# Kernel tuning notes

Hardware: AMD Instinct MI355X
Metric: run time of the kernel (lower is better)

Reference implementation:

```python
import jax, jax.numpy as jnp
import numpy as np

NEG_BIG = -1e10  # K.switch(A==0, -1e10, 0) mask value
LRELU_ALPHA = 0.2


def setup_inputs() -> dict:
    key = jax.random.key(0)
    kX, kA, kW, kS, kN = jax.random.split(key, 5)
    B, N, F, H, F_ = 4, 2048, 256, 8, 64
    X = jax.random.normal(kX, (B, N, F), dtype=jnp.float32)
    A = jax.random.bernoulli(kA, 0.05, (B, N, N)).astype(jnp.float32)
    eye = jnp.eye(N, dtype=jnp.float32)[None]
    A = jnp.maximum(A, eye)
    W = jax.random.normal(kW, (H, F, F_), dtype=jnp.float32) * 0.05
    a_self = jax.random.normal(kS, (H, F_), dtype=jnp.float32) * 0.05
    a_neigh = jax.random.normal(kN, (H, F_), dtype=jnp.float32) * 0.05
    return {"X": X, "A": A, "W": W, "a_self": a_self, "a_neigh": a_neigh}


def reference(X, A, W, a_self, a_neigh):
    # per-head linear transform, vectorized over heads: [B,H,N,F_]
    h = jnp.einsum('bnf,hfo->bhno', X, W)
    att_s = jnp.einsum('bhno,ho->bhn', h, a_self)    # attn_for_self
    att_n = jnp.einsum('bhno,ho->bhn', h, a_neigh)   # attn_for_neighs
    # broadcast-add -> dense NxN scores per head, LeakyReLU(0.2)
    dense = att_s[:, :, :, None] + att_n[:, :, None, :]          # [B,H,N,N]
    dense = jax.nn.leaky_relu(dense, LRELU_ALPHA)
    mask = jnp.where(A == 0.0, NEG_BIG, 0.0)[:, None, :, :]      # [B,1,N,N]
    attn = jax.nn.softmax(dense + mask, axis=-1)
    # weighted aggregation (dropout is identity at inference / attn_dropout=0)
    out = jnp.einsum('bhnm,bhmo->bhno', attn, h)                 # [B,H,N,F_]
    out = jax.nn.relu(out)                                       # per-head activation (concat mode)
    B, H, N, F_ = out.shape
    return out.transpose(0, 2, 1, 3).reshape(B, N, H * F_)       # concat heads
```

## Files before the change

### kernel.cpp

```cpp
#include <hip/hip_runtime.h>


constexpr int GN  = 2048;
constexpr int GHF = 512;

using sh8    = __attribute__((ext_vector_type(8))) short;
using hf8    = __attribute__((ext_vector_type(8))) _Float16;
using us4g   = __attribute__((ext_vector_type(4))) unsigned short;
using f32x4g = __attribute__((ext_vector_type(4))) float;
using u32x4g = __attribute__((ext_vector_type(4))) unsigned int;
using i32x4g = __attribute__((ext_vector_type(4))) int;

__device__ inline float gat_bf2f(unsigned short u) {
    union { unsigned int i; float f; } c; c.i = ((unsigned int)u) << 16; return c.f;
}
__device__ inline unsigned short gat_f2bf(float f) {
    union { float f; unsigned int i; } c; c.f = f;
    return (unsigned short)((c.i + 0x7fffu + ((c.i >> 16) & 1u)) >> 16);
}
__device__ inline unsigned short gat_f2h(float f) {
    _Float16 h = (_Float16)f;
    union { _Float16 h; unsigned short u; } c; c.h = h; return c.u;
}
__device__ inline float gat_h2f(unsigned short u) {
    union { _Float16 h; unsigned short u; } c; c.u = u; return (float)c.h;
}
__device__ inline int gat_isf32(const float* __restrict__ Aw) {
    float a = Aw[0];
    return (a == 0.0f) || (a == 1.0f);
}
__device__ inline unsigned int gat_enc(float f) {
    union { float f; unsigned int u; } c; c.f = f;
    return (c.u & 0x80000000u) ? ~c.u : (c.u | 0x80000000u);
}
__device__ inline float gat_dec(unsigned int e) {
    union { float f; unsigned int u; } c;
    c.u = (e & 0x80000000u) ? (e & 0x7fffffffu) : ~e;
    return c.f;
}
__device__ inline size_t gat_hswz_idx(int o, int j) {
    int jc = j >> 5, quad = (j >> 3) & 3, e = j & 7;
    int lane = quad * 16 + (o & 15);
    return (((size_t)(jc * 4 + (o >> 4))) * 64 + lane) * 8 + e;
}
__device__ inline size_t gat_wf_idx(int hh, int k, int col) {
    int kg = k >> 5, quad = (k >> 3) & 3, e = k & 7;
    int ct = col >> 4, lrw = col & 15;
    return ((((size_t)hh * 8 + kg) * 4 + ct) * 64 + (quad * 16 + lrw)) * 8 + e;
}

__global__ void GraphAttention_62981400429165_kernel() {}

constexpr size_t OFF_HS   = 256;
constexpr size_t OFF_ATTS = OFF_HS   + 8388608;
constexpr size_t OFF_EF   = OFF_ATTS + 262144;
constexpr size_t OFF_E5F  = OFF_EF   + 131072;
constexpr size_t OFF_MASK = OFF_E5F  + 131072;
constexpr size_t OFF_MAXN = OFF_MASK + 2097152;
constexpr size_t OFF_WC   = OFF_MAXN + 256;

__global__ __launch_bounds__(256) void k_mask_conv(const void* __restrict__ Araw,
                                                   const void* __restrict__ Wraw,
                                                   unsigned long long* __restrict__ mask,
                                                   unsigned int* __restrict__ maxn_enc,
                                                   unsigned short* __restrict__ Wf) {
    int tid = threadIdx.x, blk = blockIdx.x;
    int isf = gat_isf32((const float*)Araw);
    if (blk < 8192) {
        if (blk == 0 && tid < 32) maxn_enc[tid] = 0u;
        size_t i8 = ((size_t)blk * 256 + tid) * 8;
        unsigned int byte = 0;
        if (isf) {
            f32x4g v0 = *(const f32x4g*)((const float*)Araw + i8);
            f32x4g v1 = *(const f32x4g*)((const float*)Araw + i8 + 4);
#pragma unroll
            for (int e = 0; e < 4; e++) {
                byte |= (v0[e] != 0.0f ? 1u : 0u) << e;
                byte |= (v1[e] != 0.0f ? 1u : 0u) << (e + 4);
            }
        } else {
            u32x4g v = *(const u32x4g*)((const unsigned short*)Araw + i8);
#pragma unroll
            for (int w = 0; w < 4; w++) {
                byte |= ((v[w] & 0xffffu) != 0u ? 1u : 0u) << (2 * w);
                byte |= ((v[w] >> 16) != 0u ? 1u : 0u) << (2 * w + 1);
            }
        }
        ((unsigned char*)mask)[i8 >> 3] = (unsigned char)byte;
    } else {
        int gid = (blk - 8192) * 256 + tid;
        int lane = gid & 63, ct = (gid >> 6) & 3, kg = (gid >> 8) & 7, hh = gid >> 11;
        int quad = lane >> 4, lrw = lane & 15;
        int col = ct * 16 + lrw;
        us4g lo, hi;
#pragma unroll
        for (int e = 0; e < 8; e++) {
            int k = kg * 32 + quad * 8 + e;
            size_t src = (size_t)hh * 16384 + (size_t)k * 64 + col;
            unsigned short v = isf ? gat_f2bf(((const float*)Wraw)[src])
                                   : ((const unsigned short*)Wraw)[src];
            if (e < 4) lo[e] = v; else hi[e - 4] = v;
        }
        *(us4g*)&Wf[(size_t)gid * 8]     = lo;
        *(us4g*)&Wf[(size_t)gid * 8 + 4] = hi;
    }
}

constexpr int LDW = 264;
__global__ __launch_bounds__(256) void k_gemm1(const void* __restrict__ Xraw,
                                               const unsigned short* __restrict__ Wf,
                                               const void* __restrict__ aSraw,
                                               const void* __restrict__ aNraw,
                                               const float* __restrict__ Aw,
                                               unsigned short* __restrict__ hswz,
                                               float* __restrict__ att_s,
                                               unsigned short* __restrict__ Ef,
                                               unsigned short* __restrict__ E5f,
                                               unsigned int* __restrict__ maxn_enc) {
    int blk = blockIdx.x;
    int bh = blk >> 5, it = blk & 31;
    int b = bh >> 3, hh = bh & 7;
    int isf = gat_isf32(Aw);
#if defined(__gfx950__)
    __shared__ unsigned short CtT[64 * LDW];
    int wave = threadIdx.x >> 6, lane = threadIdx.x & 63;
    int lrw = lane & 15, quad = lane >> 4;
    int row0 = it * 64 + wave * 16;
    const unsigned short* wfh = Wf + (size_t)hh * 16384 + lane * 8;
    size_t xbase = ((size_t)(b * GN) + row0 + lrw) * 256;
    f32x4g acc[4] = {};
#pragma unroll 2
    for (int kg = 0; kg < 8; kg++) {
        sh8 a;
        if (isf) {
            const float* xp = (const float*)Xraw + xbase + kg * 32 + quad * 8;
            f32x4g x0 = *(const f32x4g*)xp;
            f32x4g x1 = *(const f32x4g*)(xp + 4);
            unsigned int w0_, w1_, w2_, w3_;
            asm("v_cvt_pk_bf16_f32 %0, %1, %2" : "=v"(w0_) : "v"(x0[0]), "v"(x0[1]));
            asm("v_cvt_pk_bf16_f32 %0, %1, %2" : "=v"(w1_) : "v"(x0[2]), "v"(x0[3]));
            asm("v_cvt_pk_bf16_f32 %0, %1, %2" : "=v"(w2_) : "v"(x1[0]), "v"(x1[1]));
            asm("v_cvt_pk_bf16_f32 %0, %1, %2" : "=v"(w3_) : "v"(x1[2]), "v"(x1[3]));
            i32x4g aw = {(int)w0_, (int)w1_, (int)w2_, (int)w3_};
            a = *(sh8*)&aw;
        } else {
            a = *(const sh8*)((const unsigned short*)Xraw + xbase + kg * 32 + quad * 8);
        }
        const unsigned short* wp = wfh + kg * 2048;
        sh8 w0 = *(const sh8*)&wp[0];
        sh8 w1 = *(const sh8*)&wp[512];
        sh8 w2 = *(const sh8*)&wp[1024];
        sh8 w3 = *(const sh8*)&wp[1536];
        acc[0] = __builtin_amdgcn_mfma_f32_16x16x32_bf16(a, w0, acc[0], 0, 0, 0);
        acc[1] = __builtin_amdgcn_mfma_f32_16x16x32_bf16(a, w1, acc[1], 0, 0, 0);
        acc[2] = __builtin_amdgcn_mfma_f32_16x16x32_bf16(a, w2, acc[2], 0, 0, 0);
        acc[3] = __builtin_amdgcn_mfma_f32_16x16x32_bf16(a, w3, acc[3], 0, 0, 0);
    }
    float as_l[4], an_l[4];
#pragma unroll
    for (int ct = 0; ct < 4; ct++) {
        int col = hh * 64 + ct * 16 + lrw;
        as_l[ct] = isf ? ((const float*)aSraw)[col] : gat_bf2f(((const unsigned short*)aSraw)[col]);
        an_l[ct] = isf ? ((const float*)aNraw)[col] : gat_bf2f(((const unsigned short*)aNraw)[col]);
    }
    float wmax = -3e38f;
#pragma unroll
    for (int r = 0; r < 4; r++) {
        float ps = acc[0][r] * as_l[0] + acc[1][r] * as_l[1]
                 + acc[2][r] * as_l[2] + acc[3][r] * as_l[3];
        float pn = acc[0][r] * an_l[0] + acc[1][r] * an_l[1]
                 + acc[2][r] * an_l[2] + acc[3][r] * an_l[3];
        for (int off = 1; off < 16; off <<= 1) {
            ps += __shfl_xor(ps, off);
            pn += __shfl_xor(pn, off);
        }
        int row = row0 + quad * 4 + r;
        if (lrw == 0) {
            att_s[bh * GN + row] = ps;
            float pnc = fminf(pn, 10.0f);
            Ef[bh * GN + row]  = gat_f2h(__expf(pnc));
            E5f[bh * GN + row] = gat_f2h(__expf(0.2f * pnc));
        }
        wmax = fmaxf(wmax, pn);
    }
    wmax = fmaxf(wmax, __shfl_xor(wmax, 16));
    wmax = fmaxf(wmax, __shfl_xor(wmax, 32));
    if (lane == 0) atomicMax(&maxn_enc[bh], gat_enc(wmax));
#pragma unroll
    for (int ct = 0; ct < 4; ct++) {
        int o = ct * 16 + lrw;
        int nloc = wave * 16 + quad * 4;
        us4g v;
        v[0] = gat_f2h(acc[ct][0]);
        v[1] = gat_f2h(acc[ct][1]);
        v[2] = gat_f2h(acc[ct][2]);
        v[3] = gat_f2h(acc[ct][3]);
        *(us4g*)&CtT[o * LDW + nloc] = v;
    }
    __syncthreads();
#pragma unroll
    for (int k = 0; k < 2; k++) {
        int id = k * 256 + threadIdx.x;
        int ln = id & 63, t = id >> 6;
        int jc_loc = t >> 2, ct = t & 3;
        int lrw2 = ln & 15, quad2 = ln >> 4;
        int o = ct * 16 + lrw2;
        int nloc = jc_loc * 32 + quad2 * 8;
        sh8 v = *(const sh8*)&CtT[o * LDW + nloc];
        size_t dst = ((((size_t)(bh * 64 + it * 2 + jc_loc)) * 4 + ct) * 64 + ln) * 8;
        *(sh8*)&hswz[dst] = v;
    }
#else
    if (threadIdx.x < 64) {
        int row = it * 64 + threadIdx.x;
        float hrow[64];
        for (int col = 0; col < 64; col++) {
            float sacc = 0.f;
            for (int k = 0; k < 256; k++) {
                float xv = isf ? ((const float*)Xraw)[((size_t)(b * GN) + row) * 256 + k]
                               : gat_bf2f(((const unsigned short*)Xraw)[((size_t)(b * GN) + row) * 256 + k]);
                sacc += xv * gat_bf2f(Wf[gat_wf_idx(hh, k, col)]);
            }
            hrow[col] = sacc;
        }
        size_t base = (size_t)bh * 64 * GN;
        for (int col = 0; col < 64; col++)
            hswz[base + gat_hswz_idx(col, row)] = gat_f2h(hrow[col]);
        float ps = 0.f, pn = 0.f;
        for (int col = 0; col < 64; col++) {
            float as = isf ? ((const float*)aSraw)[hh * 64 + col] : gat_bf2f(((const unsigned short*)aSraw)[hh * 64 + col]);
            float an = isf ? ((const float*)aNraw)[hh * 64 + col] : gat_bf2f(((const unsigned short*)aNraw)[hh * 64 + col]);
            ps += hrow[col] * as;
            pn += hrow[col] * an;
        }
        att_s[bh * GN + row] = ps;
        float pnc = fminf(pn, 10.0f);
        Ef[bh * GN + row]  = gat_f2h(__expf(pnc));
        E5f[bh * GN + row] = gat_f2h(__expf(0.2f * pnc));
        atomicMax(&maxn_enc[bh], gat_enc(pn));
    }
#endif
}

__global__ __launch_bounds__(256, 2) void k_attn_av(const unsigned int* __restrict__ mask32,
                                                    const unsigned short* __restrict__ hswz,
                                                    const float* __restrict__ att_s,
                                                    const unsigned short* __restrict__ Ef,
                                                    const unsigned short* __restrict__ E5f,
                                                    const unsigned int* __restrict__ maxn_enc,
                                                    const float* __restrict__ Aw,
                                                    void* __restrict__ outv) {
    int blk = blockIdx.x;
    int bh = blk & 31, it = blk >> 5;
    int b = bh >> 3, hh = bh & 7;
    int i0 = it * 64;
    int tid = threadIdx.x;
    int isf = gat_isf32(Aw);
    float maxn = gat_dec(maxn_enc[bh]);
#if defined(__gfx950__)
    int wave = tid >> 6, lane = tid & 63, lrw = lane & 15, quad = lane >> 4;
    int kq = quad * 8;
    int j0 = wave * 512;
    const unsigned short* hs = hswz + ((size_t)(bh * 64) + wave * 16) * 2048 + lane * 8;
    const unsigned int* Eu  = (const unsigned int*)Ef  + (size_t)bh * 1024;
    const unsigned int* E5u = (const unsigned int*)E5f + (size_t)bh * 1024;
    unsigned int k1p[4], k2p[4];
    const unsigned int* mrf[4];
#pragma unroll
    for (int f = 0; f < 4; f++) {
        int row = i0 + f * 16 + lrw;
        float s = att_s[bh * GN + row];
        float z = s + maxn;
        float c = fmaxf(z, 0.2f * z);
        k1p[f] = (unsigned int)gat_f2h(__expf(s - c)) * 0x00010001u;
        k2p[f] = (unsigned int)gat_f2h(__expf(0.2f * s - c)) * 0x00010001u;
        mrf[f] = mask32 + ((size_t)(b * GN) + row) * 64 + wave * 16;
    }
    f32x4g acc[4][4] = {};
    f32x4g accl[4] = {};
    hf8 ones;
#pragma unroll
    for (int e = 0; e < 8; e++) ones[e] = (_Float16)1.0f;

#pragma unroll 1
    for (int jg = 0; jg < 4; jg++) {
        u32x4g m0 = *(const u32x4g*)&mrf[0][jg * 4];
        u32x4g m1 = *(const u32x4g*)&mrf[1][jg * 4];
        u32x4g m2 = *(const u32x4g*)&mrf[2][jg * 4];
        u32x4g m3 = *(const u32x4g*)&mrf[3][jg * 4];
#pragma unroll
        for (int sj = 0; sj < 4; sj++) {
            int jc = jg * 4 + sj;
            int jh = ((j0 + jc * 32) >> 1) + quad * 4;
            u32x4g Ep  = *(const u32x4g*)&Eu[jh];
            u32x4g E5p = *(const u32x4g*)&E5u[jh];
            const unsigned short* hp = hs + jc * 2048;
            hf8 b0 = *(const hf8*)&hp[0];
            hf8 b1 = *(const hf8*)&hp[512];
            hf8 b2 = *(const hf8*)&hp[1024];
            hf8 b3 = *(const hf8*)&hp[1536];
            unsigned int wfm[4];
            wfm[0] = m0[sj] >> kq;
            wfm[1] = m1[sj] >> kq;
            wfm[2] = m2[sj] >> kq;
            wfm[3] = m3[sj] >> kq;
#pragma unroll
            for (int f = 0; f < 4; f++) {
                i32x4g fa;
#pragma unroll
                for (int pp = 0; pp < 4; pp++) {
                    unsigned int ew = Ep[pp], e5w = E5p[pp];
                    unsigned int a0, a1, mx;
                    asm("v_pk_mul_f16 %0, %1, %2" : "=v"(a0) : "v"(k1p[f]), "v"(ew));
                    asm("v_pk_mul_f16 %0, %1, %2" : "=v"(a1) : "v"(k2p[f]), "v"(e5w));
                    asm("v_pk_max_f16 %0, %1, %2" : "=v"(mx) : "v"(a0), "v"(a1));
                    unsigned int s0 = (unsigned int)__builtin_amdgcn_sbfe((int)wfm[f], 2u * pp, 1u);
                    unsigned int s1 = (unsigned int)__builtin_amdgcn_sbfe((int)wfm[f], 2u * pp + 1u, 1u);
                    fa[pp] = (int)(mx & ((s0 & 0x0000FFFFu) | (s1 & 0xFFFF0000u)));
                }
                hf8 af = *(hf8*)&fa;
                acc[f][0] = __builtin_amdgcn_mfma_f32_16x16x32_f16(af, b0, acc[f][0], 0, 0, 0);
                acc[f][1] = __builtin_amdgcn_mfma_f32_16x16x32_f16(af, b1, acc[f][1], 0, 0, 0);
                acc[f][2] = __builtin_amdgcn_mfma_f32_16x16x32_f16(af, b2, acc[f][2], 0, 0, 0);
                acc[f][3] = __builtin_amdgcn_mfma_f32_16x16x32_f16(af, b3, acc[f][3], 0, 0, 0);
                accl[f]   = __builtin_amdgcn_mfma_f32_16x16x32_f16(af, ones, accl[f], 0, 0, 0);
            }
        }
    }
    __shared__ float lred[4 * 64];
    __shared__ float lsum[64];
    __shared__ float red[4 * 4 * 16 * 17];
    if (lrw == 0) {
#pragma unroll
        for (int f = 0; f < 4; f++)
#pragma unroll
            for (int r = 0; r < 4; r++)
                lred[wave * 64 + f * 16 + quad * 4 + r] = accl[f][r];
    }
    __syncthreads();
    if (tid < 64)
        lsum[tid] = 1.0f / (lred[tid] + lred[64 + tid] + lred[128 + tid] + lred[192 + tid]);
    __syncthreads();
    for (int ct = 0; ct < 4; ct++) {
#pragma unroll
        for (int f = 0; f < 4; f++)
#pragma unroll
            for (int r = 0; r < 4; r++)
                red[((wave * 4 + f) * 16 + quad * 4 + r) * 17 + lrw] = acc[f][ct][r];
        __syncthreads();
#pragma unroll
        for (int k = 0; k < 4; k++) {
            int pos = k * 256 + tid;
            int f = pos >> 8, r16 = (pos >> 4) & 15, c16 = pos & 15;
            int bse = (f * 16 + r16) * 17 + c16;
            float sum = red[bse] + red[bse + 1088] + red[bse + 2176] + red[bse + 3264];
            float v = sum * lsum[f * 16 + r16];
            v = v > 0.f ? v : 0.f;
            int row = i0 + f * 16 + r16;
            size_t o = ((size_t)(b * GN) + row) * GHF + hh * 64 + ct * 16 + c16;
            if (isf) ((float*)outv)[o] = v;
            else     ((unsigned short*)outv)[o] = gat_f2bf(v);
        }
        __syncthreads();
    }
#else
    int row = i0 + (tid >> 2), chh = (tid & 3) * 16;
    const unsigned short* hbb = hswz + (size_t)(bh * 64) * GN;
    const unsigned int* mr = mask32 + ((size_t)(b * GN) + row) * 64;
    float s = att_s[bh * GN + row];
    float z = s + maxn;
    float c = fmaxf(z, 0.2f * z);
    unsigned short k1u = gat_f2h(__expf(s - c));
    unsigned short k2u = gat_f2h(__expf(0.2f * s - c));
    float l = 0.f;
    float accS[16] = {};
    for (int j = 0; j < GN; j++) {
        if (!((mr[j >> 5] >> (j & 31)) & 1u)) continue;
        float a0 = gat_h2f(gat_f2h(gat_h2f(k1u) * gat_h2f(Ef[(size_t)bh * GN + j])));
        float a1 = gat_h2f(gat_f2h(gat_h2f(k2u) * gat_h2f(E5f[(size_t)bh * GN + j])));
        float p = fmaxf(a0, a1);
        l += p;
        for (int cc = 0; cc < 16; cc++)
            accS[cc] += p * gat_h2f(hbb[gat_hswz_idx(chh + cc, j)]);
    }
    float li = 1.0f / l;
    for (int cc = 0; cc < 16; cc++) {
        float v = accS[cc] * li; v = v > 0.f ? v : 0.f;
        size_t oi = ((size_t)(b * GN) + row) * GHF + hh * 64 + chh + cc;
        if (isf) ((float*)outv)[oi] = v;
        else     ((unsigned short*)outv)[oi] = gat_f2bf(v);
    }
#endif
}

extern "C" void kernel_launch(void* const* d_in, const int* in_sizes, int n_in,
                              void* d_out, int out_size, void* d_ws, size_t ws_size,
                              hipStream_t stream) {
    const void* X  = d_in[0];
    const void* A  = d_in[1];
    const void* W  = d_in[2];
    const void* aS = d_in[3];
    const void* aN = d_in[4];

    char* ws = (char*)d_ws;
    unsigned short* hswz = (unsigned short*)(ws + OFF_HS);
    float* att_s = (float*)(ws + OFF_ATTS);
    unsigned short* Ef  = (unsigned short*)(ws + OFF_EF);
    unsigned short* E5f = (unsigned short*)(ws + OFF_E5F);
    unsigned long long* mask = (unsigned long long*)(ws + OFF_MASK);
    unsigned int* maxn_enc = (unsigned int*)(ws + OFF_MAXN);
    unsigned short* Wf = (unsigned short*)(ws + OFF_WC);

    k_mask_conv<<<8256, 256, 0, stream>>>(A, W, mask, maxn_enc, Wf);
    k_gemm1<<<1024, 256, 0, stream>>>(X, Wf, aS, aN, (const float*)A,
                                      hswz, att_s, Ef, E5f, maxn_enc);
    k_attn_av<<<1024, 256, 0, stream>>>((const unsigned int*)mask, hswz,
                                        att_s, Ef, E5f, maxn_enc,
                                        (const float*)A, d_out);
}
```

Before: 200.5 us.

## Fuse mask building into GEMM kernel and replace atomic max with per-block partials

The separate mask/W-conversion kernel is removed. Adjacency bitmask blocks become extra blocks of the GEMM launch. Each GEMM block now converts its head's W slice from fp32 into LDS in the swizzled layout instead of reading a prebuilt bf16 copy. The global atomicMax over encoded floats is replaced by per-block partial maxima, which the attention kernel reduces itself. This saves one launch and the atomic contention, at the cost of every GEMM block re-reading and converting its full W slice from global memory and an extra reduction in the attention kernel.

Result: faster. 176.5 us (-12.0%).

```diff
diff --git a/kernel.cpp b/kernel.cpp
--- a/kernel.cpp
+++ b/kernel.cpp
@@ -29,24 +29,10 @@
     float a = Aw[0];
     return (a == 0.0f) || (a == 1.0f);
 }
-__device__ inline unsigned int gat_enc(float f) {
-    union { float f; unsigned int u; } c; c.f = f;
-    return (c.u & 0x80000000u) ? ~c.u : (c.u | 0x80000000u);
-}
-__device__ inline float gat_dec(unsigned int e) {
-    union { float f; unsigned int u; } c;
-    c.u = (e & 0x80000000u) ? (e & 0x7fffffffu) : ~e;
-    return c.f;
-}
 __device__ inline size_t gat_hswz_idx(int o, int j) {
     int jc = j >> 5, quad = (j >> 3) & 3, e = j & 7;
     int lane = quad * 16 + (o & 15);
     return (((size_t)(jc * 4 + (o >> 4))) * 64 + lane) * 8 + e;
-}
-__device__ inline size_t gat_wf_idx(int hh, int k, int col) {
-    int kg = k >> 5, quad = (k >> 3) & 3, e = k & 7;
-    int ct = col >> 4, lrw = col & 15;
-    return ((((size_t)hh * 8 + kg) * 4 + ct) * 64 + (quad * 16 + lrw)) * 8 + e;
 }
 
 __global__ void GraphAttention_62981400429165_kernel() {}
@@ -57,83 +43,67 @@
 constexpr size_t OFF_E5F  = OFF_EF   + 131072;
 constexpr size_t OFF_MASK = OFF_E5F  + 131072;
 constexpr size_t OFF_MAXN = OFF_MASK + 2097152;
-constexpr size_t OFF_WC   = OFF_MAXN + 256;
-
-__global__ __launch_bounds__(256) void k_mask_conv(const void* __restrict__ Araw,
-                                                   const void* __restrict__ Wraw,
-                                                   unsigned long long* __restrict__ mask,
-                                                   unsigned int* __restrict__ maxn_enc,
-                                                   unsigned short* __restrict__ Wf) {
+
+constexpr int LDW = 264;
+__global__ __launch_bounds__(256) void k_gemm1(const float* __restrict__ Xraw,
+                                               const float* __restrict__ Wraw,
+                                               const float* __restrict__ aSraw,
+                                               const float* __restrict__ aNraw,
+                                               const float* __restrict__ Aw,
+                                               unsigned short* __restrict__ hswz,
+                                               float* __restrict__ att_s,
+                                               unsigned short* __restrict__ Ef,
+                                               unsigned short* __restrict__ E5f,
+                                               float* __restrict__ maxn_arr,
+                                               unsigned char* __restrict__ maskB) {
     int tid = threadIdx.x, blk = blockIdx.x;
-    int isf = gat_isf32((const float*)Araw);
-    if (blk < 8192) {
-        if (blk == 0 && tid < 32) maxn_enc[tid] = 0u;
-        size_t i8 = ((size_t)blk * 256 + tid) * 8;
+    int isf = gat_isf32(Aw);
+    if (blk >= 1024) {
+        size_t i8 = ((size_t)(blk - 1024) * 256 + tid) * 8;
         unsigned int byte = 0;
         if (isf) {
-            f32x4g v0 = *(const f32x4g*)((const float*)Araw + i8);
-            f32x4g v1 = *(const f32x4g*)((const float*)Araw + i8 + 4);
+            f32x4g v0 = *(const f32x4g*)(Aw + i8);
+            f32x4g v1 = *(const f32x4g*)(Aw + i8 + 4);
 #pragma unroll
             for (int e = 0; e < 4; e++) {
                 byte |= (v0[e] != 0.0f ? 1u : 0u) << e;
                 byte |= (v1[e] != 0.0f ? 1u : 0u) << (e + 4);
             }
         } else {
-            u32x4g v = *(const u32x4g*)((const unsigned short*)Araw + i8);
+            const unsigned short* Au = (const unsigned short*)Aw;
+            u32x4g v = *(const u32x4g*)(Au + i8);
 #pragma unroll
             for (int w = 0; w < 4; w++) {
                 byte |= ((v[w] & 0xffffu) != 0u ? 1u : 0u) << (2 * w);
                 byte |= ((v[w] >> 16) != 0u ? 1u : 0u) << (2 * w + 1);
             }
         }
-        ((unsigned char*)mask)[i8 >> 3] = (unsigned char)byte;
-    } else {
-        int gid = (blk - 8192) * 256 + tid;
-        int lane = gid & 63, ct = (gid >> 6) & 3, kg = (gid >> 8) & 7, hh = gid >> 11;
-        int quad = lane >> 4, lrw = lane & 15;
-        int col = ct * 16 + lrw;
-        us4g lo, hi;
-#pragma unroll
-        for (int e = 0; e < 8; e++) {
-            int k = kg * 32 + quad * 8 + e;
-            size_t src = (size_t)hh * 16384 + (size_t)k * 64 + col;
-            unsigned short v = isf ? gat_f2bf(((const float*)Wraw)[src])
-                                   : ((const unsigned short*)Wraw)[src];
-            if (e < 4) lo[e] = v; else hi[e - 4] = v;
-        }
-        *(us4g*)&Wf[(size_t)gid * 8]     = lo;
-        *(us4g*)&Wf[(size_t)gid * 8 + 4] = hi;
-    }
-}
-
-constexpr int LDW = 264;
-__global__ __launch_bounds__(256) void k_gemm1(const void* __restrict__ Xraw,
-                                               const unsigned short* __restrict__ Wf,
-                                               const void* __restrict__ aSraw,
-                                               const void* __restrict__ aNraw,
-                                               const float* __restrict__ Aw,
-                                               unsigned short* __restrict__ hswz,
-                                               float* __restrict__ att_s,
-                                               unsigned short* __restrict__ Ef,
-                                               unsigned short* __restrict__ E5f,
-                                               unsigned int* __restrict__ maxn_enc) {
-    int blk = blockIdx.x;
+        maskB[i8 >> 3] = (unsigned char)byte;
+        return;
+    }
     int bh = blk >> 5, it = blk & 31;
     int b = bh >> 3, hh = bh & 7;
-    int isf = gat_isf32(Aw);
 #if defined(__gfx950__)
-    __shared__ unsigned short CtT[64 * LDW];
-    int wave = threadIdx.x >> 6, lane = threadIdx.x & 63;
+    __shared__ unsigned short SH[64 * LDW];
+    int wave = tid >> 6, lane = tid & 63;
     int lrw = lane & 15, quad = lane >> 4;
+    for (int i = 0; i < 64; i++) {
+        int k = wave * 64 + i;
+        unsigned short v;
+        if (isf) v = gat_f2bf(Wraw[(size_t)hh * 16384 + k * 64 + lane]);
+        else     v = ((const unsigned short*)Wraw)[(size_t)hh * 16384 + k * 64 + lane];
+        SH[(k >> 5) * 2048 + (lane >> 4) * 512 + ((k >> 3) & 3) * 128
+           + (lane & 15) * 8 + (k & 7)] = v;
+    }
+    __syncthreads();
     int row0 = it * 64 + wave * 16;
-    const unsigned short* wfh = Wf + (size_t)hh * 16384 + lane * 8;
     size_t xbase = ((size_t)(b * GN) + row0 + lrw) * 256;
     f32x4g acc[4] = {};
 #pragma unroll 2
     for (int kg = 0; kg < 8; kg++) {
         sh8 a;
         if (isf) {
-            const float* xp = (const float*)Xraw + xbase + kg * 32 + quad * 8;
+            const float* xp = Xraw + xbase + kg * 32 + quad * 8;
             f32x4g x0 = *(const f32x4g*)xp;
             f32x4g x1 = *(const f32x4g*)(xp + 4);
             unsigned int w0_, w1_, w2_, w3_;
@@ -146,7 +116,7 @@
         } else {
             a = *(const sh8*)((const unsigned short*)Xraw + xbase + kg * 32 + quad * 8);
         }
-        const unsigned short* wp = wfh + kg * 2048;
+        const unsigned short* wp = &SH[kg * 2048 + lane * 8];
         sh8 w0 = *(const sh8*)&wp[0];
         sh8 w1 = *(const sh8*)&wp[512];
         sh8 w2 = *(const sh8*)&wp[1024];
@@ -160,8 +130,8 @@
 #pragma unroll
     for (int ct = 0; ct < 4; ct++) {
         int col = hh * 64 + ct * 16 + lrw;
-        as_l[ct] = isf ? ((const float*)aSraw)[col] : gat_bf2f(((const unsigned short*)aSraw)[col]);
-        an_l[ct] = isf ? ((const float*)aNraw)[col] : gat_bf2f(((const unsigned short*)aNraw)[col]);
+        as_l[ct] = isf ? aSraw[col] : gat_bf2f(((const unsigned short*)aSraw)[col]);
+        an_l[ct] = isf ? aNraw[col] : gat_bf2f(((const unsigned short*)aNraw)[col]);
     }
     float wmax = -3e38f;
 #pragma unroll
@@ -185,7 +155,9 @@
     }
     wmax = fmaxf(wmax, __shfl_xor(wmax, 16));
     wmax = fmaxf(wmax, __shfl_xor(wmax, 32));
-    if (lane == 0) atomicMax(&maxn_enc[bh], gat_enc(wmax));
+    if (lane == 0) maxn_arr[((bh << 5) | it) * 4 + wave] = wmax;
+    __syncthreads();
+    unsigned short* CtT = SH;
 #pragma unroll
     for (int ct = 0; ct < 4; ct++) {
         int o = ct * 16 + lrw;
@@ -200,7 +172,7 @@
     __syncthreads();
 #pragma unroll
     for (int k = 0; k < 2; k++) {
-        int id = k * 256 + threadIdx.x;
+        int id = k * 256 + tid;
         int ln = id & 63, t = id >> 6;
         int jc_loc = t >> 2, ct = t & 3;
         int lrw2 = ln & 15, quad2 = ln >> 4;
@@ -211,15 +183,19 @@
         *(sh8*)&hswz[dst] = v;
     }
 #else
-    if (threadIdx.x < 64) {
-        int row = it * 64 + threadIdx.x;
+    __shared__ float fm[256];
+    float pn_keep = -3e38f;
+    if (tid < 64) {
+        int row = it * 64 + tid;
         float hrow[64];
         for (int col = 0; col < 64; col++) {
             float sacc = 0.f;
             for (int k = 0; k < 256; k++) {
-                float xv = isf ? ((const float*)Xraw)[((size_t)(b * GN) + row) * 256 + k]
+                float xv = isf ? Xraw[((size_t)(b * GN) + row) * 256 + k]
                                : gat_bf2f(((const unsigned short*)Xraw)[((size_t)(b * GN) + row) * 256 + k]);
-                sacc += xv * gat_bf2f(Wf[gat_wf_idx(hh, k, col)]);
+                unsigned short wu = isf ? gat_f2bf(Wraw[(size_t)hh * 16384 + k * 64 + col])
+                                        : ((const unsigned short*)Wraw)[(size_t)hh * 16384 + k * 64 + col];
+                sacc += xv * gat_bf2f(wu);
             }
             hrow[col] = sacc;
         }
@@ -228,8 +204,8 @@
             hswz[base + gat_hswz_idx(col, row)] = gat_f2h(hrow[col]);
         float ps = 0.f, pn = 0.f;
         for (int col = 0; col < 64; col++) {
-            float as = isf ? ((const float*)aSraw)[hh * 64 + col] : gat_bf2f(((const unsigned short*)aSraw)[hh * 64 + col]);
-            float an = isf ? ((const float*)aNraw)[hh * 64 + col] : gat_bf2f(((const unsigned short*)aNraw)[hh * 64 + col]);
+            float as = isf ? aSraw[hh * 64 + col] : gat_bf2f(((const unsigned short*)aSraw)[hh * 64 + col]);
+            float an = isf ? aNraw[hh * 64 + col] : gat_bf2f(((const unsigned short*)aNraw)[hh * 64 + col]);
             ps += hrow[col] * as;
             pn += hrow[col] * an;
         }
@@ -237,7 +213,14 @@
         float pnc = fminf(pn, 10.0f);
         Ef[bh * GN + row]  = gat_f2h(__expf(pnc));
         E5f[bh * GN + row] = gat_f2h(__expf(0.2f * pnc));
-        atomicMax(&maxn_enc[bh], gat_enc(pn));
+        pn_keep = pn;
+    }
+    fm[tid] = pn_keep;
+    __syncthreads();
+    if (tid == 0) {
+        float m = -3e38f;
+        for (int q = 0; q < 256; q++) m = fmaxf(m, fm[q]);
+        for (int w = 0; w < 4; w++) maxn_arr[((bh << 5) | it) * 4 + w] = m;
     }
 #endif
 }
@@ -247,7 +230,7 @@
                                                     const float* __restrict__ att_s,
                                                     const unsigned short* __restrict__ Ef,
                                                     const unsigned short* __restrict__ E5f,
-                                                    const unsigned int* __restrict__ maxn_enc,
+                                                    const float* __restrict__ maxn_arr,
                                                     const float* __restrict__ Aw,
                                                     void* __restrict__ outv) {
     int blk = blockIdx.x;
@@ -256,11 +239,15 @@
     int i0 = it * 64;
     int tid = threadIdx.x;
     int isf = gat_isf32(Aw);
-    float maxn = gat_dec(maxn_enc[bh]);
 #if defined(__gfx950__)
     int wave = tid >> 6, lane = tid & 63, lrw = lane & 15, quad = lane >> 4;
     int kq = quad * 8;
     int j0 = wave * 512;
+    float mxl = -3e38f;
+    for (int q = lane; q < 128; q += 64) mxl = fmaxf(mxl, maxn_arr[bh * 128 + q]);
+#pragma unroll
+    for (int off = 1; off < 64; off <<= 1) mxl = fmaxf(mxl, __shfl_xor(mxl, off));
+    float maxn = mxl;
     const unsigned short* hs = hswz + ((size_t)(bh * 64) + wave * 16) * 2048 + lane * 8;
     const unsigned int* Eu  = (const unsigned int*)Ef  + (size_t)bh * 1024;
     const unsigned int* E5u = (const unsigned int*)E5f + (size_t)bh * 1024;
@@ -364,6 +351,8 @@
         __syncthreads();
     }
 #else
+    float maxn = -3e38f;
+    for (int q = 0; q < 128; q++) maxn = fmaxf(maxn, maxn_arr[bh * 128 + q]);
     int row = i0 + (tid >> 2), chh = (tid & 3) * 16;
     const unsigned short* hbb = hswz + (size_t)(bh * 64) * GN;
     const unsigned int* mr = mask32 + ((size_t)(b * GN) + row) * 64;
@@ -396,25 +385,23 @@
 extern "C" void kernel_launch(void* const* d_in, const int* in_sizes, int n_in,
                               void* d_out, int out_size, void* d_ws, size_t ws_size,
                               hipStream_t stream) {
-    const void* X  = d_in[0];
-    const void* A  = d_in[1];
-    const void* W  = d_in[2];
-    const void* aS = d_in[3];
-    const void* aN = d_in[4];
+    const float* X  = (const float*)d_in[0];
+    const float* A  = (const float*)d_in[1];
+    const float* W  = (const float*)d_in[2];
+    const float* aS = (const float*)d_in[3];
+    const float* aN = (const float*)d_in[4];
 
     char* ws = (char*)d_ws;
     unsigned short* hswz = (unsigned short*)(ws + OFF_HS);
     float* att_s = (float*)(ws + OFF_ATTS);
     unsigned short* Ef  = (unsigned short*)(ws + OFF_EF);
     unsigned short* E5f = (unsigned short*)(ws + OFF_E5F);
-    unsigned long long* mask = (unsigned long long*)(ws + OFF_MASK);
-    unsigned int* maxn_enc = (unsigned int*)(ws + OFF_MAXN);
-    unsigned short* Wf = (unsigned short*)(ws + OFF_WC);
-
-    k_mask_conv<<<8256, 256, 0, stream>>>(A, W, mask, maxn_enc, Wf);
-    k_gemm1<<<1024, 256, 0, stream>>>(X, Wf, aS, aN, (const float*)A,
-                                      hswz, att_s, Ef, E5f, maxn_enc);
-    k_attn_av<<<1024, 256, 0, stream>>>((const unsigned int*)mask, hswz,
-                                        att_s, Ef, E5f, maxn_enc,
-                                        (const float*)A, d_out);
-}
+    unsigned char* maskB = (unsigned char*)(ws + OFF_MASK);
+    float* maxn_arr = (float*)(ws + OFF_MAXN);
+
+    k_gemm1<<<9216, 256, 0, stream>>>(X, W, aS, aN, A,
+                                      hswz, att_s, Ef, E5f, maxn_arr, maskB);
+    k_attn_av<<<1024, 256, 0, stream>>>((const unsigned int*)maskB, hswz,
+                                        att_s, Ef, E5f, maxn_arr,
+                                        A, d_out);
+}
```
